# Optimization experiments

Measured on AMD Instinct MI355X. Metric: run time of the kernel, lower is better.

The kernel has to match this reference:

```python
import jax, jax.numpy as jnp
import numpy as np
import math

B, N, XD, ED, H = 8, 128, 256, 128, 8
DF = XD // H
FFX, FFE = 1024, 512


def _lin(x, w, b):
    return x @ w + b


def _ln(x, g, b):
    m = x.mean(-1, keepdims=True)
    v = ((x - m) ** 2).mean(-1, keepdims=True)
    return (x - m) / jnp.sqrt(v + 1e-5) * g + b


def setup_inputs() -> dict:
    key = jax.random.key(0)
    ks = jax.random.split(key, 16)
    d = {}
    d['x'] = jax.random.normal(ks[0], (B, N, XD), jnp.float32)
    d['e'] = jax.random.normal(ks[1], (B, N, N, ED), jnp.float32)
    wspecs = [('wq', (XD, XD)), ('wk', (XD, XD)), ('wv', (XD, XD)),
              ('wem', (ED, XD)), ('wea', (ED, XD)), ('wxo', (XD, XD)),
              ('weo', (XD, ED)), ('wx1', (XD, FFX)), ('wx2', (FFX, XD)),
              ('we1', (ED, FFE)), ('we2', (FFE, ED))]
    for i, (name, shp) in enumerate(wspecs):
        d[name] = jax.random.normal(ks[2 + i % 14], shp, jnp.float32) * 0.02
        d[name] = jax.random.normal(jax.random.fold_in(key, i + 10), shp, jnp.float32) * 0.02
    for name, dim in [('bq', XD), ('bk', XD), ('bv', XD), ('bem', XD), ('bea', XD),
                      ('bxo', XD), ('beo', ED), ('bx1', FFX), ('bx2', XD),
                      ('be1', FFE), ('be2', ED)]:
        d[name] = jnp.zeros((dim,), jnp.float32)
    d['gnx'] = jnp.ones((XD,), jnp.float32)
    d['bnx'] = jnp.zeros((XD,), jnp.float32)
    d['gne'] = jnp.ones((ED,), jnp.float32)
    d['bne'] = jnp.zeros((ED,), jnp.float32)
    return d


def reference(x, e, wq, wk, wv, wem, wea, wxo, weo, wx1, wx2, we1, we2,
              bq, bk, bv, bem, bea, bxo, beo, bx1, bx2, be1, be2,
              gnx, bnx, gne, bne):
    # --- NodeEdgeBlock ---
    Q = _lin(x, wq, bq).reshape(B, N, H, DF)
    K = _lin(x, wk, bk).reshape(B, N, H, DF)
    # per-channel outer product: (B, N_i, N_j, H, DF)
    Y = Q[:, :, None] * K[:, None] / math.sqrt(DF)
    E1 = _lin(e, wem, bem).reshape(B, N, N, H, DF)
    E2 = _lin(e, wea, bea).reshape(B, N, N, H, DF)
    Y = Y * (E1 + 1.0) + E2
    newE = _lin(Y.reshape(B, N, N, XD), weo, beo)
    attn = jax.nn.softmax(Y, axis=1)  # softmax over source-node axis i
    V = _lin(x, wv, bv := bv if False else bv).reshape(B, N, H, DF) if False else _lin(x, wv, bv).reshape(B, N, H, DF)
    wV = (attn * V[:, None]).sum(axis=1).reshape(B, N, XD)
    newX = _lin(wV, wxo, bxo)

    # --- FF blocks (dropout=0 => identity); note the SAME norm (norm2) is applied twice,
    # and the second residual uses the pre-norm input, matching the torch code. ---
    def ff(inp, new, w1, b1, w2, b2, g, bn):
        h = _ln(inp + new, g, bn)
        h = jax.nn.relu(_lin(h, w1, b1))
        h = _lin(h, w2, b2)
        return _ln(inp + h, g, bn)

    x_out = ff(x, newX, wx1, bx1, wx2, bx2, gnx, bnx)
    e_out = ff(e, newE, we1, be1, we2, be2, gne, bne)
    return (x_out, e_out)
```

## Files before the change

kernel.cpp:

```cpp
#include <hip/hip_runtime.h>


#define RSQRT_DF 0.17677669529663687f

typedef __attribute__((ext_vector_type(8))) short short8;
typedef __attribute__((ext_vector_type(4))) short short4v;
typedef __attribute__((ext_vector_type(4))) float f32x4;

__device__ __forceinline__ short f2bs(float f) {
    unsigned u = __float_as_uint(f);
    unsigned r = u + 0x7FFFu + ((u >> 16) & 1u);
    return (short)(r >> 16);
}
__device__ __forceinline__ float bs2f(short s) {
    return __uint_as_float(((unsigned)(unsigned short)s) << 16);
}

struct PackArgs {
    const float* W[11];
    short* Wp[11];
    int kdiv[11];
    int N[11];
    int start[12];
};

__global__ __launch_bounds__(256) void pack_all(PackArgs pa) {
    int g = blockIdx.x * 256 + threadIdx.x;
    if (g >= pa.start[11]) return;
    int i = 0;
    while (g >= pa.start[i + 1]) ++i;
    int local = g - pa.start[i];
    int kdiv = pa.kdiv[i], N = pa.N[i];
    int lane = local & 63, rest = local >> 6;
    int kb = rest % kdiv, nt = rest / kdiv;
    int n = nt * 16 + (lane & 15);
    int k0 = kb * 32 + ((lane >> 4) << 3);
    const float* W = pa.W[i];
    short8 v;
#pragma unroll
    for (int j = 0; j < 8; ++j) v[j] = f2bs(W[(size_t)(k0 + j) * N + n]);
    *(short8*)(pa.Wp[i] + (size_t)local * 8) = v;
}

__global__ __launch_bounds__(256) void qk_gemm(
    const float* __restrict__ x,
    const short* __restrict__ wqP, const short* __restrict__ wkP,
    const float* __restrict__ bq, const float* __restrict__ bk,
    float* __restrict__ Qb, float* __restrict__ Kb) {
    __shared__ short sXb[16 * 264];
    const int t = threadIdx.x, wave = t >> 6, lane = t & 63;
    const int quad = lane >> 4, l15 = lane & 15;
    const int m0 = (blockIdx.x & 63) * 16;
    const int isK = blockIdx.x >> 6;
    const short* wP = isK ? wkP : wqP;
    const float* bp = isK ? bk : bq;
    float* outp = isK ? Kb : Qb;

    const float4* x4 = (const float4*)(x + (size_t)m0 * 256);
    for (int g = t; g < 1024; g += 256) {
        float4 v = x4[g];
        int row = g >> 6, col4 = (g & 63) * 4;
        short4v sv = {f2bs(v.x), f2bs(v.y), f2bs(v.z), f2bs(v.w)};
        *(short4v*)(sXb + row * 264 + col4) = sv;
    }
    __syncthreads();

#pragma unroll 2
    for (int p = 0; p < 4; ++p) {
        int nt = wave * 4 + p;
        f32x4 acc = (f32x4){0.f, 0.f, 0.f, 0.f};
        const short* aB = sXb + l15 * 264 + quad * 8;
        const short* bB = wP + ((size_t)(nt * 8) * 64 + lane) * 8;
#pragma unroll
        for (int kb = 0; kb < 8; ++kb) {
            short8 a = *(const short8*)(aB + kb * 32);
            short8 w = *(const short8*)(bB + (size_t)kb * 512);
            acc = __builtin_amdgcn_mfma_f32_16x16x32_bf16(a, w, acc, 0, 0, 0);
        }
        int col = nt * 16 + l15;
        float bvv = bp[col];
#pragma unroll
        for (int r = 0; r < 4; ++r)
            outp[(size_t)(m0 + quad * 4 + r) * 256 + col] = acc[r] + bvv;
    }
}

__global__ __launch_bounds__(256, 3) void fused_main(
    const float* __restrict__ x, const float* __restrict__ e,
    const float* __restrict__ Qb, const float* __restrict__ Kb,
    const short* __restrict__ wvP, const short* __restrict__ wxoP,
    const short* __restrict__ wx1P, const short* __restrict__ wx2P,
    const short* __restrict__ wemP, const short* __restrict__ weaP,
    const short* __restrict__ weoP, const short* __restrict__ we1P,
    const short* __restrict__ we2P,
    const float* __restrict__ bv, const float* __restrict__ bxo,
    const float* __restrict__ bx1, const float* __restrict__ bx2,
    const float* __restrict__ bem, const float* __restrict__ bea,
    const float* __restrict__ beo, const float* __restrict__ be1,
    const float* __restrict__ be2,
    const float* __restrict__ gnx, const float* __restrict__ bnx,
    const float* __restrict__ gne, const float* __restrict__ bne,
    float* __restrict__ xout, float* __restrict__ eout) {
    __shared__ __align__(16) char ldsbuf[34304];
    const int t = threadIdx.x, wave = t >> 6, lane = t & 63;
    const int quad = lane >> 4, l15 = lane & 15;

    if (blockIdx.x < 64) {
        short* sXb  = (short*)ldsbuf;
        short* sVb  = (short*)(ldsbuf + 8448);
        short* sTbx = (short*)(ldsbuf + 16896);
        short* sRx  = (short*)(ldsbuf + 25344);
        short* sH1x = (short*)(ldsbuf + 25344);
        short* sH2x = (short*)(ldsbuf + 25344);
        const int m0 = blockIdx.x * 16;

        const float4* x4 = (const float4*)(x + (size_t)m0 * 256);
        for (int g = t; g < 1024; g += 256) {
            float4 v = x4[g];
            int row = g >> 6, col4 = (g & 63) * 4;
            short4v sv = {f2bs(v.x), f2bs(v.y), f2bs(v.z), f2bs(v.w)};
            *(short4v*)(sXb + row * 264 + col4) = sv;
        }
        __syncthreads();

        {
            short8 aX[8];
#pragma unroll
            for (int kb = 0; kb < 8; ++kb)
                aX[kb] = *(const short8*)(sXb + l15 * 264 + quad * 8 + kb * 32);
#pragma unroll
            for (int ntl = 0; ntl < 4; ++ntl) {
                int nt = wave * 4 + ntl;
                const short* bB = wvP + ((size_t)(nt * 8) * 64 + lane) * 8;
                short8 w[8];
#pragma unroll
                for (int kb = 0; kb < 8; ++kb) w[kb] = *(const short8*)(bB + (size_t)kb * 512);
                f32x4 acc = (f32x4){0.f, 0.f, 0.f, 0.f};
#pragma unroll
                for (int kb = 0; kb < 8; ++kb)
                    acc = __builtin_amdgcn_mfma_f32_16x16x32_bf16(aX[kb], w[kb], acc, 0, 0, 0);
                int col = nt * 16 + l15;
                float bvv = bv[col];
#pragma unroll
                for (int r = 0; r < 4; ++r)
                    sVb[(quad * 4 + r) * 264 + col] = f2bs(acc[r] + bvv);
            }
        }
        __syncthreads();

        {
            short8 aV[8];
#pragma unroll
            for (int kb = 0; kb < 8; ++kb)
                aV[kb] = *(const short8*)(sVb + l15 * 264 + quad * 8 + kb * 32);
#pragma unroll
            for (int ntl = 0; ntl < 4; ++ntl) {
                int nt = wave * 4 + ntl;
                const short* bB = wxoP + ((size_t)(nt * 8) * 64 + lane) * 8;
                short8 w[8];
#pragma unroll
                for (int kb = 0; kb < 8; ++kb) w[kb] = *(const short8*)(bB + (size_t)kb * 512);
                f32x4 acc = (f32x4){0.f, 0.f, 0.f, 0.f};
#pragma unroll
                for (int kb = 0; kb < 8; ++kb)
                    acc = __builtin_amdgcn_mfma_f32_16x16x32_bf16(aV[kb], w[kb], acc, 0, 0, 0);
                int col = nt * 16 + l15;
                float bvv = bxo[col];
#pragma unroll
                for (int r = 0; r < 4; ++r)
                    sRx[(quad * 4 + r) * 264 + col] = f2bs(acc[r] + bvv);
            }
        }
        __syncthreads();

        for (int rr = 0; rr < 4; ++rr) {
            int row = wave * 4 + rr;
            float v[4];
            float s1 = 0.f, s2 = 0.f;
#pragma unroll
            for (int k = 0; k < 4; ++k) {
                v[k] = bs2f(sXb[row * 264 + lane + 64 * k]) + bs2f(sRx[row * 264 + lane + 64 * k]);
                s1 += v[k]; s2 += v[k] * v[k];
            }
            for (int off = 32; off; off >>= 1) {
                s1 += __shfl_down(s1, off);
                s2 += __shfl_down(s2, off);
            }
            s1 = __shfl(s1, 0); s2 = __shfl(s2, 0);
            float mean = s1 * (1.f / 256.f);
            float var = s2 * (1.f / 256.f) - mean * mean;
            float rstd = rsqrtf(var + 1e-5f);
#pragma unroll
            for (int k = 0; k < 4; ++k)
                sTbx[row * 264 + lane + 64 * k] =
                    f2bs((v[k] - mean) * rstd * gnx[lane + 64 * k] + bnx[lane + 64 * k]);
        }
        __syncthreads();

        short8 aTx[8];
#pragma unroll
        for (int kb = 0; kb < 8; ++kb)
            aTx[kb] = *(const short8*)(sTbx + l15 * 264 + quad * 8 + kb * 32);
        f32x4 accE[4];
#pragma unroll
        for (int p = 0; p < 4; ++p) accE[p] = (f32x4){0.f, 0.f, 0.f, 0.f};

        for (int q = 0; q < 4; ++q) {
#pragma unroll
            for (int ntl = 0; ntl < 4; ++ntl) {
                int ntg = q * 16 + wave * 4 + ntl;
                const short* bB = wx1P + ((size_t)(ntg * 8) * 64 + lane) * 8;
                short8 w[8];
#pragma unroll
                for (int kb = 0; kb < 8; ++kb) w[kb] = *(const short8*)(bB + (size_t)kb * 512);
                f32x4 acc = (f32x4){0.f, 0.f, 0.f, 0.f};
#pragma unroll
                for (int kb = 0; kb < 8; ++kb)
                    acc = __builtin_amdgcn_mfma_f32_16x16x32_bf16(aTx[kb], w[kb], acc, 0, 0, 0);
                int coll = (wave * 4 + ntl) * 16 + l15;
                float bvv = bx1[ntg * 16 + l15];
#pragma unroll
                for (int r = 0; r < 4; ++r)
                    sH1x[(quad * 4 + r) * 264 + coll] = f2bs(fmaxf(acc[r] + bvv, 0.f));
            }
            __syncthreads();
            {
                short8 aHx[8];
#pragma unroll
                for (int kb = 0; kb < 8; ++kb)
                    aHx[kb] = *(const short8*)(sH1x + l15 * 264 + quad * 8 + kb * 32);
#pragma unroll
                for (int ntl = 0; ntl < 4; ++ntl) {
                    int nt = wave * 4 + ntl;
                    const short* bB = wx2P + ((size_t)(nt * 32 + q * 8) * 64 + lane) * 8;
                    short8 w[8];
#pragma unroll
                    for (int kb = 0; kb < 8; ++kb) w[kb] = *(const short8*)(bB + (size_t)kb * 512);
#pragma unroll
                    for (int kb = 0; kb < 8; ++kb)
                        accE[ntl] = __builtin_amdgcn_mfma_f32_16x16x32_bf16(aHx[kb], w[kb], accE[ntl], 0, 0, 0);
                }
            }
            __syncthreads();
        }
#pragma unroll
        for (int ntl = 0; ntl < 4; ++ntl) {
            int col = (wave * 4 + ntl) * 16 + l15;
            float bvv = bx2[col];
#pragma unroll
            for (int r = 0; r < 4; ++r)
                sH2x[(quad * 4 + r) * 264 + col] = f2bs(accE[ntl][r] + bvv);
        }
        __syncthreads();

        for (int rr = 0; rr < 4; ++rr) {
            int row = wave * 4 + rr;
            float v[4];
            float s1 = 0.f, s2 = 0.f;
#pragma unroll
            for (int k = 0; k < 4; ++k) {
                v[k] = bs2f(sXb[row * 264 + lane + 64 * k]) + bs2f(sH2x[row * 264 + lane + 64 * k]);
                s1 += v[k]; s2 += v[k] * v[k];
            }
            for (int off = 32; off; off >>= 1) {
                s1 += __shfl_down(s1, off);
                s2 += __shfl_down(s2, off);
            }
            s1 = __shfl(s1, 0); s2 = __shfl(s2, 0);
            float mean = s1 * (1.f / 256.f);
            float var = s2 * (1.f / 256.f) - mean * mean;
            float rstd = rsqrtf(var + 1e-5f);
#pragma unroll
            for (int k = 0; k < 4; ++k)
                xout[(size_t)(m0 + row) * 256 + lane + 64 * k] =
                    (v[k] - mean) * rstd * gnx[lane + 64 * k] + bnx[lane + 64 * k];
        }
        return;
    }

    short* sEb = (short*)ldsbuf;
    short* sYb = (short*)(ldsbuf + 8704);
    short* sTb = (short*)(ldsbuf + 8704);
    float* sH2 = (float*)(ldsbuf + 8704);
    short* sR  = (short*)(ldsbuf + 25600);
    short* sH1 = (short*)(ldsbuf + 25600);

    const int r0 = (blockIdx.x - 64) * 32;
    const int b = r0 >> 14;
    const int j0 = r0 & 127;

    float g0 = gne[lane], g1 = gne[lane + 64];
    float bn0 = bne[lane], bn1 = bne[lane + 64];

    float qk[2][4][4];
#pragma unroll
    for (int ntl = 0; ntl < 4; ++ntl) {
        const int col = (wave * 4 + ntl) * 16 + l15;
        const float q = Qb[(size_t)(r0 >> 7) * 256 + col] * RSQRT_DF;
#pragma unroll
        for (int mt = 0; mt < 2; ++mt) {
            const float* kp = Kb + (size_t)((b << 7) + j0 + mt * 16 + quad * 4) * 256 + col;
#pragma unroll
            for (int r = 0; r < 4; ++r) qk[mt][ntl][r] = q * kp[(size_t)r * 256];
        }
    }

    {
        const float4* e4 = (const float4*)(e + (size_t)r0 * 128);
        for (int g = t; g < 1024; g += 256) {
            float4 v = e4[g];
            int row = g >> 5, col4 = (g & 31) * 4;
            short4v sv = {f2bs(v.x), f2bs(v.y), f2bs(v.z), f2bs(v.w)};
            *(short4v*)(sEb + row * 136 + col4) = sv;
        }
    }
    __syncthreads();

    {
        short8 aE[2][4];
#pragma unroll
        for (int mt = 0; mt < 2; ++mt)
#pragma unroll
            for (int kb = 0; kb < 4; ++kb)
                aE[mt][kb] = *(const short8*)(sEb + (mt * 16 + l15) * 136 + quad * 8 + kb * 32);
#pragma unroll
        for (int ntl = 0; ntl < 4; ++ntl) {
            const int nt = wave * 4 + ntl;
            const short* b1 = wemP + ((size_t)(nt * 4) * 64 + lane) * 8;
            const short* b2 = weaP + ((size_t)(nt * 4) * 64 + lane) * 8;
            short8 w1[4], w2[4];
#pragma unroll
            for (int kb = 0; kb < 4; ++kb) {
                w1[kb] = *(const short8*)(b1 + (size_t)kb * 512);
                w2[kb] = *(const short8*)(b2 + (size_t)kb * 512);
            }
            const int col = nt * 16 + l15;
            const float bm = bem[col], ba = bea[col];
#pragma unroll
            for (int mt = 0; mt < 2; ++mt) {
                f32x4 a1 = (f32x4){0.f, 0.f, 0.f, 0.f};
                f32x4 a2 = (f32x4){0.f, 0.f, 0.f, 0.f};
#pragma unroll
                for (int kb = 0; kb < 4; ++kb) {
                    a1 = __builtin_amdgcn_mfma_f32_16x16x32_bf16(aE[mt][kb], w1[kb], a1, 0, 0, 0);
                    a2 = __builtin_amdgcn_mfma_f32_16x16x32_bf16(aE[mt][kb], w2[kb], a2, 0, 0, 0);
                }
#pragma unroll
                for (int r = 0; r < 4; ++r) {
                    int row = mt * 16 + quad * 4 + r;
                    float y = qk[mt][ntl][r] * (a1[r] + bm + 1.0f) + (a2[r] + ba);
                    sYb[row * 264 + col] = f2bs(y);
                }
            }
        }
    }
    __syncthreads();

    {
        short8 aY[2][8];
#pragma unroll
        for (int mt = 0; mt < 2; ++mt)
#pragma unroll
            for (int kb = 0; kb < 8; ++kb)
                aY[mt][kb] = *(const short8*)(sYb + (mt * 16 + l15) * 264 + quad * 8 + kb * 32);
#pragma unroll
        for (int ntl = 0; ntl < 2; ++ntl) {
            const int nt = wave * 2 + ntl;
            const short* bB = weoP + ((size_t)(nt * 8) * 64 + lane) * 8;
            short8 w[8];
#pragma unroll
            for (int kb = 0; kb < 8; ++kb) w[kb] = *(const short8*)(bB + (size_t)kb * 512);
            const int col = nt * 16 + l15;
            const float bo = beo[col];
#pragma unroll
            for (int mt = 0; mt < 2; ++mt) {
                f32x4 acc = (f32x4){0.f, 0.f, 0.f, 0.f};
#pragma unroll
                for (int kb = 0; kb < 8; ++kb)
                    acc = __builtin_amdgcn_mfma_f32_16x16x32_bf16(aY[mt][kb], w[kb], acc, 0, 0, 0);
#pragma unroll
                for (int r = 0; r < 4; ++r)
                    sR[(mt * 16 + quad * 4 + r) * 136 + col] = f2bs(acc[r] + bo);
            }
        }
    }
    __syncthreads();

    for (int rr = 0; rr < 8; ++rr) {
        int row = wave * 8 + rr;
        float v0 = bs2f(sEb[row * 136 + lane]) + bs2f(sR[row * 136 + lane]);
        float v1 = bs2f(sEb[row * 136 + lane + 64]) + bs2f(sR[row * 136 + lane + 64]);
        float s1 = v0 + v1, s2 = v0 * v0 + v1 * v1;
        for (int off = 32; off; off >>= 1) {
            s1 += __shfl_down(s1, off);
            s2 += __shfl_down(s2, off);
        }
        s1 = __shfl(s1, 0); s2 = __shfl(s2, 0);
        float mean = s1 * 0.0078125f;
        float var = s2 * 0.0078125f - mean * mean;
        float rstd = rsqrtf(var + 1e-5f);
        sTb[row * 136 + lane]      = f2bs((v0 - mean) * rstd * g0 + bn0);
        sTb[row * 136 + lane + 64] = f2bs((v1 - mean) * rstd * g1 + bn1);
    }
    __syncthreads();

    short8 aT[2][4];
#pragma unroll
    for (int mt = 0; mt < 2; ++mt)
#pragma unroll
        for (int kb = 0; kb < 4; ++kb)
            aT[mt][kb] = *(const short8*)(sTb + (mt * 16 + l15) * 136 + quad * 8 + kb * 32);
    f32x4 accE[4];
#pragma unroll
    for (int p = 0; p < 4; ++p) accE[p] = (f32x4){0.f, 0.f, 0.f, 0.f};

    for (int q = 0; q < 4; ++q) {
#pragma unroll
        for (int ntl = 0; ntl < 2; ++ntl) {
            const int ntg = q * 8 + wave * 2 + ntl;
            const short* bB = we1P + ((size_t)(ntg * 4) * 64 + lane) * 8;
            short8 w[4];
#pragma unroll
            for (int kb = 0; kb < 4; ++kb) w[kb] = *(const short8*)(bB + (size_t)kb * 512);
            const int coll = (wave * 2 + ntl) * 16 + l15;
            const float bvv = be1[ntg * 16 + l15];
#pragma unroll
            for (int mt = 0; mt < 2; ++mt) {
                f32x4 acc = (f32x4){0.f, 0.f, 0.f, 0.f};
#pragma unroll
                for (int kb = 0; kb < 4; ++kb)
                    acc = __builtin_amdgcn_mfma_f32_16x16x32_bf16(aT[mt][kb], w[kb], acc, 0, 0, 0);
#pragma unroll
                for (int r = 0; r < 4; ++r)
                    sH1[(mt * 16 + quad * 4 + r) * 136 + coll] = f2bs(fmaxf(acc[r] + bvv, 0.f));
            }
        }
        __syncthreads();
        {
            short8 aH[2][4];
#pragma unroll
            for (int mt = 0; mt < 2; ++mt)
#pragma unroll
                for (int kb = 0; kb < 4; ++kb)
                    aH[mt][kb] = *(const short8*)(sH1 + (mt * 16 + l15) * 136 + quad * 8 + kb * 32);
#pragma unroll
            for (int ntl = 0; ntl < 2; ++ntl) {
                const int nt = wave * 2 + ntl;
                const short* bB = we2P + ((size_t)(nt * 16 + q * 4) * 64 + lane) * 8;
                short8 w[4];
#pragma unroll
                for (int kb = 0; kb < 4; ++kb) w[kb] = *(const short8*)(bB + (size_t)kb * 512);
#pragma unroll
                for (int mt = 0; mt < 2; ++mt) {
#pragma unroll
                    for (int kb = 0; kb < 4; ++kb)
                        accE[ntl * 2 + mt] = __builtin_amdgcn_mfma_f32_16x16x32_bf16(
                            aH[mt][kb], w[kb], accE[ntl * 2 + mt], 0, 0, 0);
                }
            }
        }
        __syncthreads();
    }
#pragma unroll
    for (int ntl = 0; ntl < 2; ++ntl)
#pragma unroll
        for (int mt = 0; mt < 2; ++mt) {
            const int col = (wave * 2 + ntl) * 16 + l15;
            const float bvv = be2[col];
#pragma unroll
            for (int r = 0; r < 4; ++r)
                sH2[(mt * 16 + quad * 4 + r) * 132 + col] = accE[ntl * 2 + mt][r] + bvv;
        }
    __syncthreads();

    for (int rr = 0; rr < 8; ++rr) {
        int row = wave * 8 + rr;
        float v0 = bs2f(sEb[row * 136 + lane]) + sH2[row * 132 + lane];
        float v1 = bs2f(sEb[row * 136 + lane + 64]) + sH2[row * 132 + lane + 64];
        float s1 = v0 + v1, s2 = v0 * v0 + v1 * v1;
        for (int off = 32; off; off >>= 1) {
            s1 += __shfl_down(s1, off);
            s2 += __shfl_down(s2, off);
        }
        s1 = __shfl(s1, 0); s2 = __shfl(s2, 0);
        float mean = s1 * 0.0078125f;
        float var = s2 * 0.0078125f - mean * mean;
        float rstd = rsqrtf(var + 1e-5f);
        size_t o = (size_t)(r0 + row) * 128;
        eout[o + lane]      = (v0 - mean) * rstd * g0 + bn0;
        eout[o + lane + 64] = (v1 - mean) * rstd * g1 + bn1;
    }
}

extern "C" void kernel_launch(void* const* d_in, const int* in_sizes, int n_in,
                              void* d_out, int out_size, void* d_ws, size_t ws_size,
                              hipStream_t stream) {
    const float* x   = (const float*)d_in[0];
    const float* e   = (const float*)d_in[1];
    const float* wq  = (const float*)d_in[2];
    const float* wk  = (const float*)d_in[3];
    const float* wv  = (const float*)d_in[4];
    const float* wem = (const float*)d_in[5];
    const float* wea = (const float*)d_in[6];
    const float* wxo = (const float*)d_in[7];
    const float* weo = (const float*)d_in[8];
    const float* wx1 = (const float*)d_in[9];
    const float* wx2 = (const float*)d_in[10];
    const float* we1 = (const float*)d_in[11];
    const float* we2 = (const float*)d_in[12];
    const float* bq  = (const float*)d_in[13];
    const float* bk  = (const float*)d_in[14];
    const float* bv  = (const float*)d_in[15];
    const float* bem = (const float*)d_in[16];
    const float* bea = (const float*)d_in[17];
    const float* bxo = (const float*)d_in[18];
    const float* beo = (const float*)d_in[19];
    const float* bx1 = (const float*)d_in[20];
    const float* bx2 = (const float*)d_in[21];
    const float* be1 = (const float*)d_in[22];
    const float* be2 = (const float*)d_in[23];
    const float* gnx = (const float*)d_in[24];
    const float* bnx = (const float*)d_in[25];
    const float* gne = (const float*)d_in[26];
    const float* bne = (const float*)d_in[27];

    float* out = (float*)d_out;

    float* ws = (float*)d_ws;
    float* Qb = ws;
    float* Kb = Qb + 262144;
    short* base = (short*)(Kb + 262144);
    short* wqP  = base;
    short* wkP  = wqP + 65536;
    short* wvP  = wkP + 65536;
    short* wxoP = wvP + 65536;
    short* wx1P = wxoP + 65536;
    short* wx2P = wx1P + 262144;
    short* wemP = wx2P + 262144;
    short* weaP = wemP + 32768;
    short* weoP = weaP + 32768;
    short* we1P = weoP + 32768;
    short* we2P = we1P + 65536;

    PackArgs pa;
    const float* Ws[11] = {wq, wk, wv, wxo, wx1, wx2, wem, wea, weo, we1, we2};
    short* Wps[11] = {wqP, wkP, wvP, wxoP, wx1P, wx2P, wemP, weaP, weoP, we1P, we2P};
    int Ks[11] = {256, 256, 256, 256, 256, 1024, 128, 128, 256, 128, 512};
    int Ns[11] = {256, 256, 256, 256, 1024, 256, 256, 256, 128, 512, 128};
    int acc = 0;
    for (int i = 0; i < 11; ++i) {
        pa.W[i] = Ws[i];
        pa.Wp[i] = Wps[i];
        pa.kdiv[i] = Ks[i] >> 5;
        pa.N[i] = Ns[i];
        pa.start[i] = acc;
        acc += (Ns[i] >> 4) * (Ks[i] >> 5) * 64;
    }
    pa.start[11] = acc;
    pack_all<<<(acc + 255) / 256, 256, 0, stream>>>(pa);

    qk_gemm<<<128, 256, 0, stream>>>(x, wqP, wkP, bq, bk, Qb, Kb);

    fused_main<<<4160, 256, 0, stream>>>(
        x, e, Qb, Kb, wvP, wxoP, wx1P, wx2P, wemP, weaP, weoP, we1P, we2P,
        bv, bxo, bx1, bx2, bem, bea, beo, be1, be2,
        gnx, bnx, gne, bne, out, out + 262144);
}
```

Baseline: 283.5 us.

## Double rows per block to amortize weight fetches across more MFMA tiles

The fused kernel moves to 512-thread blocks, each handling twice as many rows: 64 edge rows and 32 node rows. The grid halves and LDS per block doubles. Each wave now reuses its loaded weight fragments across more row tiles, which cuts global/L2 weight traffic per output row. A-operand fragments are now read from LDS inside the MFMA loops rather than held in registers. The Q·K scale is computed inline rather than precomputed. The trade-off is higher LDS use per block and a tighter register budget under launch_bounds(512,3), which risks spills or lower occupancy.

```diff
diff --git a/kernel.cpp b/kernel.cpp
--- a/kernel.cpp
+++ b/kernel.cpp
@@ -85,7 +85,7 @@
     }
 }
 
-__global__ __launch_bounds__(256, 3) void fused_main(
+__global__ __launch_bounds__(512, 3) void fused_main(
     const float* __restrict__ x, const float* __restrict__ e,
     const float* __restrict__ Qb, const float* __restrict__ Kb,
     const short* __restrict__ wvP, const short* __restrict__ wxoP,
@@ -101,21 +101,21 @@
     const float* __restrict__ gnx, const float* __restrict__ bnx,
     const float* __restrict__ gne, const float* __restrict__ bne,
     float* __restrict__ xout, float* __restrict__ eout) {
-    __shared__ __align__(16) char ldsbuf[34304];
+    __shared__ __align__(16) char ldsbuf[68608];
     const int t = threadIdx.x, wave = t >> 6, lane = t & 63;
     const int quad = lane >> 4, l15 = lane & 15;
 
-    if (blockIdx.x < 64) {
+    if (blockIdx.x < 32) {
         short* sXb  = (short*)ldsbuf;
-        short* sVb  = (short*)(ldsbuf + 8448);
-        short* sTbx = (short*)(ldsbuf + 16896);
-        short* sRx  = (short*)(ldsbuf + 25344);
-        short* sH1x = (short*)(ldsbuf + 25344);
-        short* sH2x = (short*)(ldsbuf + 25344);
-        const int m0 = blockIdx.x * 16;
+        short* sVb  = (short*)(ldsbuf + 16896);
+        short* sTbx = (short*)(ldsbuf + 33792);
+        short* sRx  = (short*)(ldsbuf + 50688);
+        short* sH1x = (short*)(ldsbuf + 50688);
+        short* sH2x = (short*)(ldsbuf + 50688);
+        const int m0 = blockIdx.x * 32;
 
         const float4* x4 = (const float4*)(x + (size_t)m0 * 256);
-        for (int g = t; g < 1024; g += 256) {
+        for (int g = t; g < 2048; g += 512) {
             float4 v = x4[g];
             int row = g >> 6, col4 = (g & 63) * 4;
             short4v sv = {f2bs(v.x), f2bs(v.y), f2bs(v.z), f2bs(v.w)};
@@ -123,52 +123,50 @@
         }
         __syncthreads();
 
-        {
-            short8 aX[8];
-#pragma unroll
-            for (int kb = 0; kb < 8; ++kb)
-                aX[kb] = *(const short8*)(sXb + l15 * 264 + quad * 8 + kb * 32);
-#pragma unroll
-            for (int ntl = 0; ntl < 4; ++ntl) {
-                int nt = wave * 4 + ntl;
-                const short* bB = wvP + ((size_t)(nt * 8) * 64 + lane) * 8;
-                short8 w[8];
-#pragma unroll
-                for (int kb = 0; kb < 8; ++kb) w[kb] = *(const short8*)(bB + (size_t)kb * 512);
+#pragma unroll
+        for (int ntl = 0; ntl < 2; ++ntl) {
+            const int nt = wave * 2 + ntl;
+            const short* bB = wvP + ((size_t)(nt * 8) * 64 + lane) * 8;
+            short8 w[8];
+#pragma unroll
+            for (int kb = 0; kb < 8; ++kb) w[kb] = *(const short8*)(bB + (size_t)kb * 512);
+            const int col = nt * 16 + l15;
+            const float bvv = bv[col];
+#pragma unroll
+            for (int mt = 0; mt < 2; ++mt) {
                 f32x4 acc = (f32x4){0.f, 0.f, 0.f, 0.f};
 #pragma unroll
-                for (int kb = 0; kb < 8; ++kb)
-                    acc = __builtin_amdgcn_mfma_f32_16x16x32_bf16(aX[kb], w[kb], acc, 0, 0, 0);
-                int col = nt * 16 + l15;
-                float bvv = bv[col];
+                for (int kb = 0; kb < 8; ++kb) {
+                    short8 a = *(const short8*)(sXb + (mt * 16 + l15) * 264 + quad * 8 + kb * 32);
+                    acc = __builtin_amdgcn_mfma_f32_16x16x32_bf16(a, w[kb], acc, 0, 0, 0);
+                }
 #pragma unroll
                 for (int r = 0; r < 4; ++r)
-                    sVb[(quad * 4 + r) * 264 + col] = f2bs(acc[r] + bvv);
-            }
-        }
-        __syncthreads();
-
-        {
-            short8 aV[8];
-#pragma unroll
-            for (int kb = 0; kb < 8; ++kb)
-                aV[kb] = *(const short8*)(sVb + l15 * 264 + quad * 8 + kb * 32);
-#pragma unroll
-            for (int ntl = 0; ntl < 4; ++ntl) {
-                int nt = wave * 4 + ntl;
-                const short* bB = wxoP + ((size_t)(nt * 8) * 64 + lane) * 8;
-                short8 w[8];
-#pragma unroll
-                for (int kb = 0; kb < 8; ++kb) w[kb] = *(const short8*)(bB + (size_t)kb * 512);
+                    sVb[(mt * 16 + quad * 4 + r) * 264 + col] = f2bs(acc[r] + bvv);
+            }
+        }
+        __syncthreads();
+
+#pragma unroll
+        for (int ntl = 0; ntl < 2; ++ntl) {
+            const int nt = wave * 2 + ntl;
+            const short* bB = wxoP + ((size_t)(nt * 8) * 64 + lane) * 8;
+            short8 w[8];
+#pragma unroll
+            for (int kb = 0; kb < 8; ++kb) w[kb] = *(const short8*)(bB + (size_t)kb * 512);
+            const int col = nt * 16 + l15;
+            const float bvv = bxo[col];
+#pragma unroll
+            for (int mt = 0; mt < 2; ++mt) {
                 f32x4 acc = (f32x4){0.f, 0.f, 0.f, 0.f};
 #pragma unroll
-                for (int kb = 0; kb < 8; ++kb)
-                    acc = __builtin_amdgcn_mfma_f32_16x16x32_bf16(aV[kb], w[kb], acc, 0, 0, 0);
-                int col = nt * 16 + l15;
-                float bvv = bxo[col];
+                for (int kb = 0; kb < 8; ++kb) {
+                    short8 a = *(const short8*)(sVb + (mt * 16 + l15) * 264 + quad * 8 + kb * 32);
+                    acc = __builtin_amdgcn_mfma_f32_16x16x32_bf16(a, w[kb], acc, 0, 0, 0);
+                }
 #pragma unroll
                 for (int r = 0; r < 4; ++r)
-                    sRx[(quad * 4 + r) * 264 + col] = f2bs(acc[r] + bvv);
+                    sRx[(mt * 16 + quad * 4 + r) * 264 + col] = f2bs(acc[r] + bvv);
             }
         }
         __syncthreads();
@@ -197,60 +195,64 @@
         }
         __syncthreads();
 
-        short8 aTx[8];
-#pragma unroll
-        for (int kb = 0; kb < 8; ++kb)
-            aTx[kb] = *(const short8*)(sTbx + l15 * 264 + quad * 8 + kb * 32);
-        f32x4 accE[4];
-#pragma unroll
-        for (int p = 0; p < 4; ++p) accE[p] = (f32x4){0.f, 0.f, 0.f, 0.f};
+        f32x4 accEx[2][2];
+#pragma unroll
+        for (int i = 0; i < 2; ++i)
+#pragma unroll
+            for (int j = 0; j < 2; ++j) accEx[i][j] = (f32x4){0.f, 0.f, 0.f, 0.f};
 
         for (int q = 0; q < 4; ++q) {
 #pragma unroll
-            for (int ntl = 0; ntl < 4; ++ntl) {
-                int ntg = q * 16 + wave * 4 + ntl;
+            for (int ntl = 0; ntl < 2; ++ntl) {
+                const int ntg = q * 16 + wave * 2 + ntl;
                 const short* bB = wx1P + ((size_t)(ntg * 8) * 64 + lane) * 8;
                 short8 w[8];
 #pragma unroll
                 for (int kb = 0; kb < 8; ++kb) w[kb] = *(const short8*)(bB + (size_t)kb * 512);
-                f32x4 acc = (f32x4){0.f, 0.f, 0.f, 0.f};
-#pragma unroll
-                for (int kb = 0; kb < 8; ++kb)
-                    acc = __builtin_amdgcn_mfma_f32_16x16x32_bf16(aTx[kb], w[kb], acc, 0, 0, 0);
-                int coll = (wave * 4 + ntl) * 16 + l15;
-                float bvv = bx1[ntg * 16 + l15];
+                const int coll = (wave * 2 + ntl) * 16 + l15;
+                const float bvv = bx1[ntg * 16 + l15];
+#pragma unroll
+                for (int mt = 0; mt < 2; ++mt) {
+                    f32x4 acc = (f32x4){0.f, 0.f, 0.f, 0.f};
+#pragma unroll
+                    for (int kb = 0; kb < 8; ++kb) {
+                        short8 a = *(const short8*)(sTbx + (mt * 16 + l15) * 264 + quad * 8 + kb * 32);
+                        acc = __builtin_amdgcn_mfma_f32_16x16x32_bf16(a, w[kb], acc, 0, 0, 0);
+                    }
+#pragma unroll
+                    for (int r = 0; r < 4; ++r)
+                        sH1x[(mt * 16 + quad * 4 + r) * 264 + coll] = f2bs(fmaxf(acc[r] + bvv, 0.f));
+                }
+            }
+            __syncthreads();
+#pragma unroll
+            for (int ntl = 0; ntl < 2; ++ntl) {
+                const int nt = wave * 2 + ntl;
+                const short* bB = wx2P + ((size_t)(nt * 32 + q * 8) * 64 + lane) * 8;
+                short8 w[8];
+#pragma unroll
+                for (int kb = 0; kb < 8; ++kb) w[kb] = *(const short8*)(bB + (size_t)kb * 512);
+#pragma unroll
+                for (int mt = 0; mt < 2; ++mt) {
+#pragma unroll
+                    for (int kb = 0; kb < 8; ++kb) {
+                        short8 a = *(const short8*)(sH1x + (mt * 16 + l15) * 264 + quad * 8 + kb * 32);
+                        accEx[ntl][mt] = __builtin_amdgcn_mfma_f32_16x16x32_bf16(a, w[kb], accEx[ntl][mt], 0, 0, 0);
+                    }
+                }
+            }
+            __syncthreads();
+        }
+#pragma unroll
+        for (int ntl = 0; ntl < 2; ++ntl)
+#pragma unroll
+            for (int mt = 0; mt < 2; ++mt) {
+                const int col = (wave * 2 + ntl) * 16 + l15;
+                const float bvv = bx2[col];
 #pragma unroll
                 for (int r = 0; r < 4; ++r)
-                    sH1x[(quad * 4 + r) * 264 + coll] = f2bs(fmaxf(acc[r] + bvv, 0.f));
-            }
-            __syncthreads();
-            {
-                short8 aHx[8];
-#pragma unroll
-                for (int kb = 0; kb < 8; ++kb)
-                    aHx[kb] = *(const short8*)(sH1x + l15 * 264 + quad * 8 + kb * 32);
-#pragma unroll
-                for (int ntl = 0; ntl < 4; ++ntl) {
-                    int nt = wave * 4 + ntl;
-                    const short* bB = wx2P + ((size_t)(nt * 32 + q * 8) * 64 + lane) * 8;
-                    short8 w[8];
-#pragma unroll
-                    for (int kb = 0; kb < 8; ++kb) w[kb] = *(const short8*)(bB + (size_t)kb * 512);
-#pragma unroll
-                    for (int kb = 0; kb < 8; ++kb)
-                        accE[ntl] = __builtin_amdgcn_mfma_f32_16x16x32_bf16(aHx[kb], w[kb], accE[ntl], 0, 0, 0);
-                }
-            }
-            __syncthreads();
-        }
-#pragma unroll
-        for (int ntl = 0; ntl < 4; ++ntl) {
-            int col = (wave * 4 + ntl) * 16 + l15;
-            float bvv = bx2[col];
-#pragma unroll
-            for (int r = 0; r < 4; ++r)
-                sH2x[(quad * 4 + r) * 264 + col] = f2bs(accE[ntl][r] + bvv);
-        }
+                    sH2x[(mt * 16 + quad * 4 + r) * 264 + col] = f2bs(accEx[ntl][mt][r] + bvv);
+            }
         __syncthreads();
 
         for (int rr = 0; rr < 4; ++rr) {
@@ -279,35 +281,19 @@
     }
 
     short* sEb = (short*)ldsbuf;
-    short* sYb = (short*)(ldsbuf + 8704);
-    short* sTb = (short*)(ldsbuf + 8704);
-    float* sH2 = (float*)(ldsbuf + 8704);
-    short* sR  = (short*)(ldsbuf + 25600);
-    short* sH1 = (short*)(ldsbuf + 25600);
-
-    const int r0 = (blockIdx.x - 64) * 32;
+    short* sYb = (short*)(ldsbuf + 17408);
+    short* sTb = (short*)(ldsbuf + 17408);
+    float* sH2 = (float*)(ldsbuf + 17408);
+    short* sR  = (short*)(ldsbuf + 51200);
+    short* sH1 = (short*)(ldsbuf + 51200);
+
+    const int r0 = (blockIdx.x - 32) * 64;
     const int b = r0 >> 14;
     const int j0 = r0 & 127;
 
-    float g0 = gne[lane], g1 = gne[lane + 64];
-    float bn0 = bne[lane], bn1 = bne[lane + 64];
-
-    float qk[2][4][4];
-#pragma unroll
-    for (int ntl = 0; ntl < 4; ++ntl) {
-        const int col = (wave * 4 + ntl) * 16 + l15;
-        const float q = Qb[(size_t)(r0 >> 7) * 256 + col] * RSQRT_DF;
-#pragma unroll
-        for (int mt = 0; mt < 2; ++mt) {
-            const float* kp = Kb + (size_t)((b << 7) + j0 + mt * 16 + quad * 4) * 256 + col;
-#pragma unroll
-            for (int r = 0; r < 4; ++r) qk[mt][ntl][r] = q * kp[(size_t)r * 256];
-        }
-    }
-
     {
         const float4* e4 = (const float4*)(e + (size_t)r0 * 128);
-        for (int g = t; g < 1024; g += 256) {
+        for (int g = t; g < 2048; g += 512) {
             float4 v = e4[g];
             int row = g >> 5, col4 = (g & 31) * 4;
             short4v sv = {f2bs(v.x), f2bs(v.y), f2bs(v.z), f2bs(v.w)};
@@ -316,120 +302,110 @@
     }
     __syncthreads();
 
+#pragma unroll
+    for (int ntl = 0; ntl < 2; ++ntl) {
+        const int nt = wave * 2 + ntl;
+        const short* b1 = wemP + ((size_t)(nt * 4) * 64 + lane) * 8;
+        const short* b2 = weaP + ((size_t)(nt * 4) * 64 + lane) * 8;
+        short8 w1[4], w2[4];
+#pragma unroll
+        for (int kb = 0; kb < 4; ++kb) {
+            w1[kb] = *(const short8*)(b1 + (size_t)kb * 512);
+            w2[kb] = *(const short8*)(b2 + (size_t)kb * 512);
+        }
+        const int col = nt * 16 + l15;
+        const float bm = bem[col], ba = bea[col];
+        const float q = Qb[(size_t)(r0 >> 7) * 256 + col] * RSQRT_DF;
+#pragma unroll
+        for (int mt = 0; mt < 4; ++mt) {
+            const float* kp = Kb + (size_t)((b << 7) + j0 + mt * 16 + quad * 4) * 256 + col;
+            float kv[4];
+#pragma unroll
+            for (int r = 0; r < 4; ++r) kv[r] = kp[(size_t)r * 256];
+            f32x4 a1 = (f32x4){0.f, 0.f, 0.f, 0.f};
+            f32x4 a2 = (f32x4){0.f, 0.f, 0.f, 0.f};
+#pragma unroll
+            for (int kb = 0; kb < 4; ++kb) {
+                short8 a = *(const short8*)(sEb + (mt * 16 + l15) * 136 + quad * 8 + kb * 32);
+                a1 = __builtin_amdgcn_mfma_f32_16x16x32_bf16(a, w1[kb], a1, 0, 0, 0);
+                a2 = __builtin_amdgcn_mfma_f32_16x16x32_bf16(a, w2[kb], a2, 0, 0, 0);
+            }
+#pragma unroll
+            for (int r = 0; r < 4; ++r) {
+                int row = mt * 16 + quad * 4 + r;
+                float y = q * kv[r] * (a1[r] + bm + 1.0f) + (a2[r] + ba);
+                sYb[row * 264 + col] = f2bs(y);
+            }
+        }
+    }
+    __syncthreads();
+
     {
-        short8 aE[2][4];
-#pragma unroll
-        for (int mt = 0; mt < 2; ++mt)
-#pragma unroll
-            for (int kb = 0; kb < 4; ++kb)
-                aE[mt][kb] = *(const short8*)(sEb + (mt * 16 + l15) * 136 + quad * 8 + kb * 32);
-#pragma unroll
-        for (int ntl = 0; ntl < 4; ++ntl) {
-            const int nt = wave * 4 + ntl;
-            const short* b1 = wemP + ((size_t)(nt * 4) * 64 + lane) * 8;
-            const short* b2 = weaP + ((size_t)(nt * 4) * 64 + lane) * 8;
-            short8 w1[4], w2[4];
-#pragma unroll
-            for (int kb = 0; kb < 4; ++kb) {
-                w1[kb] = *(const short8*)(b1 + (size_t)kb * 512);
-                w2[kb] = *(const short8*)(b2 + (size_t)kb * 512);
-            }
-            const int col = nt * 16 + l15;
-            const float bm = bem[col], ba = bea[col];
-#pragma unroll
-            for (int mt = 0; mt < 2; ++mt) {
-                f32x4 a1 = (f32x4){0.f, 0.f, 0.f, 0.f};
-                f32x4 a2 = (f32x4){0.f, 0.f, 0.f, 0.f};
-#pragma unroll
-                for (int kb = 0; kb < 4; ++kb) {
-                    a1 = __builtin_amdgcn_mfma_f32_16x16x32_bf16(aE[mt][kb], w1[kb], a1, 0, 0, 0);
-                    a2 = __builtin_amdgcn_mfma_f32_16x16x32_bf16(aE[mt][kb], w2[kb], a2, 0, 0, 0);
-                }
-#pragma unroll
-                for (int r = 0; r < 4; ++r) {
-                    int row = mt * 16 + quad * 4 + r;
-                    float y = qk[mt][ntl][r] * (a1[r] + bm + 1.0f) + (a2[r] + ba);
-                    sYb[row * 264 + col] = f2bs(y);
-                }
-            }
+        const int nt = wave;
+        const short* bB = weoP + ((size_t)(nt * 8) * 64 + lane) * 8;
+        short8 w[8];
+#pragma unroll
+        for (int kb = 0; kb < 8; ++kb) w[kb] = *(const short8*)(bB + (size_t)kb * 512);
+        const int col = nt * 16 + l15;
+        const float bo = beo[col];
+#pragma unroll
+        for (int mt = 0; mt < 4; ++mt) {
+            f32x4 acc = (f32x4){0.f, 0.f, 0.f, 0.f};
+#pragma unroll
+            for (int kb = 0; kb < 8; ++kb) {
+                short8 a = *(const short8*)(sYb + (mt * 16 + l15) * 264 + quad * 8 + kb * 32);
+                acc = __builtin_amdgcn_mfma_f32_16x16x32_bf16(a, w[kb], acc, 0, 0, 0);
+            }
+#pragma unroll
+            for (int r = 0; r < 4; ++r)
+                sR[(mt * 16 + quad * 4 + r) * 136 + col] = f2bs(acc[r] + bo);
         }
     }
     __syncthreads();
 
     {
-        short8 aY[2][8];
-#pragma unroll
-        for (int mt = 0; mt < 2; ++mt)
-#pragma unroll
-            for (int kb = 0; kb < 8; ++kb)
-                aY[mt][kb] = *(const short8*)(sYb + (mt * 16 + l15) * 264 + quad * 8 + kb * 32);
-#pragma unroll
-        for (int ntl = 0; ntl < 2; ++ntl) {
-            const int nt = wave * 2 + ntl;
-            const short* bB = weoP + ((size_t)(nt * 8) * 64 + lane) * 8;
-            short8 w[8];
-#pragma unroll
-            for (int kb = 0; kb < 8; ++kb) w[kb] = *(const short8*)(bB + (size_t)kb * 512);
-            const int col = nt * 16 + l15;
-            const float bo = beo[col];
-#pragma unroll
-            for (int mt = 0; mt < 2; ++mt) {
-                f32x4 acc = (f32x4){0.f, 0.f, 0.f, 0.f};
-#pragma unroll
-                for (int kb = 0; kb < 8; ++kb)
-                    acc = __builtin_amdgcn_mfma_f32_16x16x32_bf16(aY[mt][kb], w[kb], acc, 0, 0, 0);
-#pragma unroll
-                for (int r = 0; r < 4; ++r)
-                    sR[(mt * 16 + quad * 4 + r) * 136 + col] = f2bs(acc[r] + bo);
-            }
+        float g0 = gne[lane], g1 = gne[lane + 64];
+        float bn0 = bne[lane], bn1 = bne[lane + 64];
+        for (int rr = 0; rr < 8; ++rr) {
+            int row = wave * 8 + rr;
+            float v0 = bs2f(sEb[row * 136 + lane]) + bs2f(sR[row * 136 + lane]);
+            float v1 = bs2f(sEb[row * 136 + lane + 64]) + bs2f(sR[row * 136 + lane + 64]);
+            float s1 = v0 + v1, s2 = v0 * v0 + v1 * v1;
+            for (int off = 32; off; off >>= 1) {
+                s1 += __shfl_down(s1, off);
+                s2 += __shfl_down(s2, off);
+            }
+            s1 = __shfl(s1, 0); s2 = __shfl(s2, 0);
+            float mean = s1 * 0.0078125f;
+            float var = s2 * 0.0078125f - mean * mean;
+            float rstd = rsqrtf(var + 1e-5f);
+            sTb[row * 136 + lane]      = f2bs((v0 - mean) * rstd * g0 + bn0);
+            sTb[row * 136 + lane + 64] = f2bs((v1 - mean) * rstd * g1 + bn1);
         }
     }
     __syncthreads();
 
-    for (int rr = 0; rr < 8; ++rr) {
-        int row = wave * 8 + rr;
-        float v0 = bs2f(sEb[row * 136 + lane]) + bs2f(sR[row * 136 + lane]);
-        float v1 = bs2f(sEb[row * 136 + lane + 64]) + bs2f(sR[row * 136 + lane + 64]);
-        float s1 = v0 + v1, s2 = v0 * v0 + v1 * v1;
-        for (int off = 32; off; off >>= 1) {
-            s1 += __shfl_down(s1, off);
-            s2 += __shfl_down(s2, off);
-        }
-        s1 = __shfl(s1, 0); s2 = __shfl(s2, 0);
-        float mean = s1 * 0.0078125f;
-        float var = s2 * 0.0078125f - mean * mean;
-        float rstd = rsqrtf(var + 1e-5f);
-        sTb[row * 136 + lane]      = f2bs((v0 - mean) * rstd * g0 + bn0);
-        sTb[row * 136 + lane + 64] = f2bs((v1 - mean) * rstd * g1 + bn1);
-    }
-    __syncthreads();
-
-    short8 aT[2][4];
-#pragma unroll
-    for (int mt = 0; mt < 2; ++mt)
-#pragma unroll
-        for (int kb = 0; kb < 4; ++kb)
-            aT[mt][kb] = *(const short8*)(sTb + (mt * 16 + l15) * 136 + quad * 8 + kb * 32);
     f32x4 accE[4];
 #pragma unroll
     for (int p = 0; p < 4; ++p) accE[p] = (f32x4){0.f, 0.f, 0.f, 0.f};
 
     for (int q = 0; q < 4; ++q) {
-#pragma unroll
-        for (int ntl = 0; ntl < 2; ++ntl) {
-            const int ntg = q * 8 + wave * 2 + ntl;
+        {
+            const int ntg = q * 8 + wave;
             const short* bB = we1P + ((size_t)(ntg * 4) * 64 + lane) * 8;
             short8 w[4];
 #pragma unroll
             for (int kb = 0; kb < 4; ++kb) w[kb] = *(const short8*)(bB + (size_t)kb * 512);
-            const int coll = (wave * 2 + ntl) * 16 + l15;
+            const int coll = wave * 16 + l15;
             const float bvv = be1[ntg * 16 + l15];
 #pragma unroll
-            for (int mt = 0; mt < 2; ++mt) {
+            for (int mt = 0; mt < 4; ++mt) {
                 f32x4 acc = (f32x4){0.f, 0.f, 0.f, 0.f};
 #pragma unroll
-                for (int kb = 0; kb < 4; ++kb)
-                    acc = __builtin_amdgcn_mfma_f32_16x16x32_bf16(aT[mt][kb], w[kb], acc, 0, 0, 0);
+                for (int kb = 0; kb < 4; ++kb) {
+                    short8 a = *(const short8*)(sTb + (mt * 16 + l15) * 136 + quad * 8 + kb * 32);
+                    acc = __builtin_amdgcn_mfma_f32_16x16x32_bf16(a, w[kb], acc, 0, 0, 0);
+                }
 #pragma unroll
                 for (int r = 0; r < 4; ++r)
                     sH1[(mt * 16 + quad * 4 + r) * 136 + coll] = f2bs(fmaxf(acc[r] + bvv, 0.f));
@@ -437,58 +413,53 @@
         }
         __syncthreads();
         {
-            short8 aH[2][4];
-#pragma unroll
-            for (int mt = 0; mt < 2; ++mt)
-#pragma unroll
-                for (int kb = 0; kb < 4; ++kb)
-                    aH[mt][kb] = *(const short8*)(sH1 + (mt * 16 + l15) * 136 + quad * 8 + kb * 32);
-#pragma unroll
-            for (int ntl = 0; ntl < 2; ++ntl) {
-                const int nt = wave * 2 + ntl;
-                const short* bB = we2P + ((size_t)(nt * 16 + q * 4) * 64 + lane) * 8;
-                short8 w[4];
-#pragma unroll
-                for (int kb = 0; kb < 4; ++kb) w[kb] = *(const short8*)(bB + (size_t)kb * 512);
-#pragma unroll
-                for (int mt = 0; mt < 2; ++mt) {
-#pragma unroll
-                    for (int kb = 0; kb < 4; ++kb)
-                        accE[ntl * 2 + mt] = __builtin_amdgcn_mfma_f32_16x16x32_bf16(
-                            aH[mt][kb], w[kb], accE[ntl * 2 + mt], 0, 0, 0);
+            const int nt = wave;
+            const short* bB = we2P + ((size_t)(nt * 16 + q * 4) * 64 + lane) * 8;
+            short8 w[4];
+#pragma unroll
+            for (int kb = 0; kb < 4; ++kb) w[kb] = *(const short8*)(bB + (size_t)kb * 512);
+#pragma unroll
+            for (int mt = 0; mt < 4; ++mt) {
+#pragma unroll
+                for (int kb = 0; kb < 4; ++kb) {
+                    short8 a = *(const short8*)(sH1 + (mt * 16 + l15) * 136 + quad * 8 + kb * 32);
+                    accE[mt] = __builtin_amdgcn_mfma_f32_16x16x32_bf16(a, w[kb], accE[mt], 0, 0, 0);
                 }
             }
         }
         __syncthreads();
     }
-#pragma unroll
-    for (int ntl = 0; ntl < 2; ++ntl)
-#pragma unroll
-        for (int mt = 0; mt < 2; ++mt) {
-            const int col = (wave * 2 + ntl) * 16 + l15;
-            const float bvv = be2[col];
+    {
+        const int col = wave * 16 + l15;
+        const float bvv = be2[col];
+#pragma unroll
+        for (int mt = 0; mt < 4; ++mt)
 #pragma unroll
             for (int r = 0; r < 4; ++r)
-                sH2[(mt * 16 + quad * 4 + r) * 132 + col] = accE[ntl * 2 + mt][r] + bvv;
-        }
+                sH2[(mt * 16 + quad * 4 + r) * 132 + col] = accE[mt][r] + bvv;
+    }
     __syncthreads();
 
-    for (int rr = 0; rr < 8; ++rr) {
-        int row = wave * 8 + rr;
-        float v0 = bs2f(sEb[row * 136 + lane]) + sH2[row * 132 + lane];
-        float v1 = bs2f(sEb[row * 136 + lane + 64]) + sH2[row * 132 + lane + 64];
-        float s1 = v0 + v1, s2 = v0 * v0 + v1 * v1;
-        for (int off = 32; off; off >>= 1) {
-            s1 += __shfl_down(s1, off);
-            s2 += __shfl_down(s2, off);
-        }
-        s1 = __shfl(s1, 0); s2 = __shfl(s2, 0);
-        float mean = s1 * 0.0078125f;
-        float var = s2 * 0.0078125f - mean * mean;
-        float rstd = rsqrtf(var + 1e-5f);
-        size_t o = (size_t)(r0 + row) * 128;
-        eout[o + lane]      = (v0 - mean) * rstd * g0 + bn0;
-        eout[o + lane + 64] = (v1 - mean) * rstd * g1 + bn1;
+    {
+        float g0 = gne[lane], g1 = gne[lane + 64];
+        float bn0 = bne[lane], bn1 = bne[lane + 64];
+        for (int rr = 0; rr < 8; ++rr) {
+            int row = wave * 8 + rr;
+            float v0 = bs2f(sEb[row * 136 + lane]) + sH2[row * 132 + lane];
+            float v1 = bs2f(sEb[row * 136 + lane + 64]) + sH2[row * 132 + lane + 64];
+            float s1 = v0 + v1, s2 = v0 * v0 + v1 * v1;
+            for (int off = 32; off; off >>= 1) {
+                s1 += __shfl_down(s1, off);
+                s2 += __shfl_down(s2, off);
+            }
+            s1 = __shfl(s1, 0); s2 = __shfl(s2, 0);
+            float mean = s1 * 0.0078125f;
+            float var = s2 * 0.0078125f - mean * mean;
+            float rstd = rsqrtf(var + 1e-5f);
+            size_t o = (size_t)(r0 + row) * 128;
+            eout[o + lane]      = (v0 - mean) * rstd * g0 + bn0;
+            eout[o + lane + 64] = (v1 - mean) * rstd * g1 + bn1;
+        }
     }
 }
 
@@ -561,7 +532,7 @@
 
     qk_gemm<<<128, 256, 0, stream>>>(x, wqP, wkP, bq, bk, Qb, Kb);
 
-    fused_main<<<4160, 256, 0, stream>>>(
+    fused_main<<<2080, 512, 0, stream>>>(
         x, e, Qb, Kb, wvP, wxoP, wx1P, wx2P, wemP, weaP, weoP, we1P, we2P,
         bv, bxo, bx1, bx2, bem, bea, beo, be1, be2,
         gnx, bnx, gne, bne, out, out + 262144);
```

Result: slower. 296.8 us (+4.7%).
